# Optimization experiments

Measured on AMD Instinct MI355X. Metric: run time of the kernel, lower is better.

Reference implementation:

```python
import jax, jax.numpy as jnp
import numpy as np

B, L, D = 2, 2048, 1024
H, G = 16, 2            # num_heads, num_kv_groups
HPG = H // G            # heads per kv group = 8
DQK, DV = 128, 128      # qk_head_dim, v_head_dim (head_dim=64, ratios=2.0)


def setup_inputs() -> dict:
    key = jax.random.key(0)
    ks = jax.random.split(key, 12)

    def xavier(k, shape, scale=1.0):
        fan_in, fan_out = shape[0], shape[1]
        lim = np.sqrt(6.0 / (fan_in + fan_out))
        return jax.random.uniform(k, shape, jnp.float32, -lim, lim) * scale

    return {
        "in_q": jax.random.normal(ks[0], (B, L, D), jnp.float32),
        "in_k": jax.random.normal(ks[1], (B, L, D), jnp.float32),
        "in_v": jax.random.normal(ks[2], (B, L, D), jnp.float32),
        # weights stored as [in, out] (transpose of torch Linear); qk_init_scale=0.5
        "Wq": xavier(ks[3], (D, H * DQK), 0.5),
        "bq": jnp.zeros((H * DQK,), jnp.float32),
        "Wk": xavier(ks[4], (D, G * DQK), 0.5),
        "bk": jnp.zeros((G * DQK,), jnp.float32),
        "Wv": xavier(ks[5], (D, G * DV)),
        "bv": jnp.zeros((G * DV,), jnp.float32),
        "Wo": xavier(ks[6], (H * DV, D)),
        "bo": jnp.zeros((D,), jnp.float32),
        "q_extra_scale": jnp.ones((1,), jnp.float32),
    }


def reference(in_q, in_k, in_v, Wq, bq, Wk, bk, Wv, bv, Wo, bo, q_extra_scale):
    # fused projections
    q = (in_q @ Wq + bq) * q_extra_scale              # [B,L,H*DQK]
    k = in_k @ Wk + bk                                 # [B,L,G*DQK]
    v = in_v @ Wv + bv                                 # [B,L,G*DV]

    # reshape: keep GQA group structure instead of materializing repeat_interleave
    q = q.reshape(B, L, G, HPG, DQK)                   # heads grouped: head h = g*HPG + m
    k = k.reshape(B, L, G, DQK)
    v = v.reshape(B, L, G, DV)

    scale = 1.0 / np.sqrt(DQK)
    # scores: [B,G,HPG,L_q,L_kv]
    scores = jnp.einsum("bsgmd,btgd->bgmst", q, k) * scale
    causal = jnp.tril(jnp.ones((L, L), bool))          # is_causal=True
    scores = jnp.where(causal, scores, jnp.finfo(scores.dtype).min)
    attn = jax.nn.softmax(scores, axis=-1)
    ctx = jnp.einsum("bgmst,btgd->bsgmd", attn, v)     # [B,L,G,HPG,DV]
    ctx = ctx.reshape(B, L, H * DV)
    return ctx @ Wo + bo                               # [B,L,D]
```

## Files before the change

### kernel.cpp

```cpp
#include <hip/hip_runtime.h>


typedef __bf16 bf16;
typedef __bf16 bf16x8 __attribute__((ext_vector_type(8)));
typedef __bf16 bf16x4 __attribute__((ext_vector_type(4)));
typedef float f32x4 __attribute__((ext_vector_type(4)));
typedef float float4v __attribute__((ext_vector_type(4)));

#define MFMA_BF16(a, b, c) __builtin_amdgcn_mfma_f32_16x16x32_bf16((a), (b), (c), 0, 0, 0)

static constexpr int Bz = 2, Lz = 2048, Dz = 1024;
static constexpr int Hz = 16, Gz = 2;
static constexpr int DQKz = 128, DVz = 128;

__device__ __forceinline__ void async_copy16(const bf16* g, bf16* l) {
    __builtin_amdgcn_global_load_lds(
        (const __attribute__((address_space(1))) unsigned int*)g,
        (__attribute__((address_space(3))) unsigned int*)l, 16, 0, 0);
}

__global__ __launch_bounds__(256) void cvt3(
    const float* __restrict__ q, const float* __restrict__ k,
    const float* __restrict__ v, bf16* __restrict__ dq,
    bf16* __restrict__ dk, bf16* __restrict__ dv)
{
    const float* s = blockIdx.y == 0 ? q : (blockIdx.y == 1 ? k : v);
    bf16* d = blockIdx.y == 0 ? dq : (blockIdx.y == 1 ? dk : dv);
    int i = (blockIdx.x * 256 + threadIdx.x) * 8;
    float4v a = *(const float4v*)(s + i);
    float4v b = *(const float4v*)(s + i + 4);
    bf16x8 o;
    #pragma unroll
    for (int j = 0; j < 4; ++j) { o[j] = (bf16)a[j]; o[j + 4] = (bf16)b[j]; }
    *(bf16x8*)(d + i) = o;
}

__global__ __launch_bounds__(256) void wtrans4(
    const float* __restrict__ W0, bf16* __restrict__ T0,
    const float* __restrict__ W1, bf16* __restrict__ T1,
    const float* __restrict__ W2, bf16* __restrict__ T2,
    const float* __restrict__ W3, bf16* __restrict__ T3)
{
    const float* W; bf16* WT; int K, N;
    switch (blockIdx.z) {
        case 0:  W = W0; WT = T0; K = 1024; N = 2048; break;
        case 1:  W = W1; WT = T1; K = 1024; N = 256;  break;
        case 2:  W = W2; WT = T2; K = 1024; N = 256;  break;
        default: W = W3; WT = T3; K = 2048; N = 1024; break;
    }
    int tiles_n = N >> 5, tiles_k = K >> 5;
    int linear = blockIdx.x + blockIdx.y * 64;
    if (linear >= tiles_n * tiles_k) return;
    int n0 = (linear % tiles_n) * 32, k0 = (linear / tiles_n) * 32;

    __shared__ bf16 t[32][33];
    int tx = threadIdx.x & 31, ty = threadIdx.x >> 5;
    #pragma unroll
    for (int i = 0; i < 4; ++i)
        t[ty + i * 8][tx] = (bf16)W[(size_t)(k0 + ty + i * 8) * N + n0 + tx];
    __syncthreads();
    #pragma unroll
    for (int i = 0; i < 4; ++i)
        WT[(size_t)(n0 + ty + i * 8) * K + k0 + tx] = t[tx][ty + i * 8];
}

template <typename TC>
__global__ __launch_bounds__(256, 3) void gemm128(
    const bf16* __restrict__ A, const bf16* __restrict__ BT,
    const float* __restrict__ bias, const float* __restrict__ scale_ptr,
    float scale_const, TC* __restrict__ C, int M, int N, int K)
{
    __shared__ bf16 As[128 * 64];
    __shared__ bf16 Bs[128 * 64];

    const int tid  = threadIdx.x;
    const int wave = tid >> 6;
    const int lane = tid & 63;
    const int quad = lane >> 4;
    const int l16  = lane & 15;
    const int sw   = l16 & 7;
    const int wm = wave >> 1, wn = wave & 1;
    const int m0 = blockIdx.y * 128;
    const int n0 = blockIdx.x * 128;

    f32x4 acc[4][4] = {};

    for (int k0 = 0; k0 < K; k0 += 64) {
        #pragma unroll
        for (int s = 0; s < 4; ++s) {
            int i = s * 256 + tid;
            int row = i >> 3, c = (i & 7) ^ (row & 7);
            async_copy16(A + (size_t)(m0 + row) * K + k0 + c * 8, &As[(size_t)i * 8]);
        }
        #pragma unroll
        for (int s = 0; s < 4; ++s) {
            int i = s * 256 + tid;
            int row = i >> 3, c = (i & 7) ^ (row & 7);
            async_copy16(BT + (size_t)(n0 + row) * K + k0 + c * 8, &Bs[(size_t)i * 8]);
        }
        __syncthreads();

        #pragma unroll
        for (int ks = 0; ks < 2; ++ks) {
            bf16x8 af[4], bfv[4];
            #pragma unroll
            for (int mt = 0; mt < 4; ++mt)
                af[mt] = *(const bf16x8*)(&As[((wm * 64 + mt * 16 + l16) * 8
                                               + ((ks * 4 + quad) ^ sw)) * 8]);
            #pragma unroll
            for (int nt = 0; nt < 4; ++nt)
                bfv[nt] = *(const bf16x8*)(&Bs[((wn * 64 + nt * 16 + l16) * 8
                                                + ((ks * 4 + quad) ^ sw)) * 8]);
            #pragma unroll
            for (int mt = 0; mt < 4; ++mt)
                #pragma unroll
                for (int nt = 0; nt < 4; ++nt)
                    acc[mt][nt] = MFMA_BF16(af[mt], bfv[nt], acc[mt][nt]);
        }
        __syncthreads();
    }

    const float scale = (scale_ptr ? scale_ptr[0] : 1.0f) * scale_const;
    #pragma unroll
    for (int nt = 0; nt < 4; ++nt) {
        int col = n0 + wn * 64 + nt * 16 + l16;
        float bv = bias[col];
        #pragma unroll
        for (int mt = 0; mt < 4; ++mt)
            #pragma unroll
            for (int r = 0; r < 4; ++r) {
                int row = m0 + wm * 64 + mt * 16 + quad * 4 + r;
                C[(size_t)row * N + col] = (TC)((acc[mt][nt][r] + bv) * scale);
            }
    }
}

__global__ __launch_bounds__(256, 4) void gemm64_kv(
    const bf16* __restrict__ A0, const bf16* __restrict__ BT0,
    const float* __restrict__ bias0, bf16* __restrict__ C0,
    const bf16* __restrict__ A1, const bf16* __restrict__ BT1,
    const float* __restrict__ bias1, bf16* __restrict__ C1,
    int M, int N, int K)
{
    const bool isV = blockIdx.z == 1;
    const bf16* A  = isV ? A1 : A0;
    const bf16* BT = isV ? BT1 : BT0;
    const float* bias = isV ? bias1 : bias0;
    bf16* C = isV ? C1 : C0;

    __shared__ bf16 As[64 * 64];
    __shared__ bf16 Bs[64 * 64];

    const int tid  = threadIdx.x;
    const int wave = tid >> 6;
    const int lane = tid & 63;
    const int quad = lane >> 4;
    const int l16  = lane & 15;
    const int sw   = l16 & 7;
    const int m0 = blockIdx.y * 64;
    const int n0 = blockIdx.x * 64;

    f32x4 acc[4] = {};

    for (int k0 = 0; k0 < K; k0 += 64) {
        #pragma unroll
        for (int s = 0; s < 2; ++s) {
            int i = s * 256 + tid;
            int row = i >> 3, c = (i & 7) ^ (row & 7);
            async_copy16(A + (size_t)(m0 + row) * K + k0 + c * 8, &As[(size_t)i * 8]);
        }
        #pragma unroll
        for (int s = 0; s < 2; ++s) {
            int i = s * 256 + tid;
            int row = i >> 3, c = (i & 7) ^ (row & 7);
            async_copy16(BT + (size_t)(n0 + row) * K + k0 + c * 8, &Bs[(size_t)i * 8]);
        }
        __syncthreads();

        #pragma unroll
        for (int ks = 0; ks < 2; ++ks) {
            bf16x8 af = *(const bf16x8*)(&As[((wave * 16 + l16) * 8
                                              + ((ks * 4 + quad) ^ sw)) * 8]);
            #pragma unroll
            for (int nf = 0; nf < 4; ++nf) {
                bf16x8 bfv = *(const bf16x8*)(&Bs[((nf * 16 + l16) * 8
                                                   + ((ks * 4 + quad) ^ sw)) * 8]);
                acc[nf] = MFMA_BF16(af, bfv, acc[nf]);
            }
        }
        __syncthreads();
    }

    #pragma unroll
    for (int nf = 0; nf < 4; ++nf) {
        int col = n0 + nf * 16 + l16;
        float bv = bias[col];
        #pragma unroll
        for (int r = 0; r < 4; ++r) {
            int row = m0 + wave * 16 + quad * 4 + r;
            float v = acc[nf][r] + bv;
            if (isV) C[(size_t)col * M + row] = (bf16)v;
            else     C[(size_t)row * N + col] = (bf16)v;
        }
    }
}

__global__ __launch_bounds__(256, 2) void attn_fused(
    const bf16* __restrict__ Q,
    const bf16* __restrict__ Kp,
    const bf16* __restrict__ VT,
    bf16* __restrict__ ctx)
{
    __shared__ bf16 Kb[2][64 * 128];
    __shared__ bf16 Vb[2][128 * 64];
    __shared__ bf16 Ps[4 * 16 * 68];

    const int tid  = threadIdx.x;
    const int wave = tid >> 6;
    const int lane = tid & 63;
    const int quad = lane >> 4;
    const int l16  = lane & 15;
    const int sw   = l16 & 7;

    const int h  = blockIdx.y;
    const int b  = blockIdx.z;
    const int g  = h >> 3;

    const bf16* kgbase = Kp + (size_t)(b * Lz) * (Gz * DQKz) + g * DQKz;
    const bf16* vgbase = VT + (size_t)(g * DVz) * (Bz * Lz) + b * Lz;

    auto stage = [&](int kt, int buf) {
        const bf16* kb = kgbase + (size_t)(kt * 64) * (Gz * DQKz);
        #pragma unroll
        for (int s = 0; s < 4; ++s) {
            int i = s * 256 + tid;
            int key = i >> 4, c = (i & 15) ^ (key & 7);
            async_copy16(kb + (size_t)key * (Gz * DQKz) + c * 8,
                         &Kb[buf][(size_t)i * 8]);
        }
        const bf16* vb = vgbase + kt * 64;
        #pragma unroll
        for (int s = 0; s < 4; ++s) {
            int i = s * 256 + tid;
            int dv = i >> 3, c = (i & 7) ^ (dv & 7);
            async_copy16(vb + (size_t)dv * (Bz * Lz) + c * 8,
                         &Vb[buf][(size_t)i * 8]);
        }
    };

    for (int pass = 0; pass < 2; ++pass) {
        const int qt  = pass == 0 ? (31 - blockIdx.x) : blockIdx.x;
        const int q0  = qt * 64;
        const int nkt = qt + 1;

        bf16x8 qf[4];
        {
            const int qrow = q0 + wave * 16 + l16;
            const bf16* qbase = Q + (size_t)(b * Lz + qrow) * (Hz * DQKz) + h * DQKz;
            #pragma unroll
            for (int ks = 0; ks < 4; ++ks)
                qf[ks] = *(const bf16x8*)(qbase + ks * 32 + quad * 8);
        }

        f32x4 oacc[8] = {};
        float lrow[4] = {0.0f, 0.0f, 0.0f, 0.0f};

        if (pass) __syncthreads();
        stage(0, 0);
        int cur = 0;

        for (int kt = 0; kt < nkt; ++kt) {
            __syncthreads();
            if (kt + 1 < nkt) stage(kt + 1, cur ^ 1);

            const bf16* kcur = Kb[cur];
            const bf16* vcur = Vb[cur];

            f32x4 sacc[4] = {};
            #pragma unroll
            for (int nf = 0; nf < 4; ++nf) {
                #pragma unroll
                for (int ks = 0; ks < 4; ++ks) {
                    bf16x8 kf = *(const bf16x8*)(&kcur[((nf * 16 + l16) * 16
                                                        + ((ks * 4 + quad) ^ sw)) * 8]);
                    sacc[nf] = MFMA_BF16(qf[ks], kf, sacc[nf]);
                }
            }

            float pv[4][4];
            if (kt == nkt - 1) {
                const int kv0 = kt * 64;
                #pragma unroll
                for (int nf = 0; nf < 4; ++nf) {
                    int col = kv0 + nf * 16 + l16;
                    #pragma unroll
                    for (int r = 0; r < 4; ++r) {
                        int row = q0 + wave * 16 + quad * 4 + r;
                        pv[nf][r] = (col > row) ? 0.0f : exp2f(sacc[nf][r] - 8.0f);
                    }
                }
            } else {
                #pragma unroll
                for (int nf = 0; nf < 4; ++nf)
                    #pragma unroll
                    for (int r = 0; r < 4; ++r)
                        pv[nf][r] = exp2f(sacc[nf][r] - 8.0f);
            }

            #pragma unroll
            for (int r = 0; r < 4; ++r)
                lrow[r] += (pv[0][r] + pv[1][r]) + (pv[2][r] + pv[3][r]);

            bf16* ps = &Ps[wave * 16 * 68];
            #pragma unroll
            for (int nf = 0; nf < 4; ++nf)
                #pragma unroll
                for (int r = 0; r < 4; ++r)
                    ps[(quad * 4 + r) * 68 + nf * 16 + l16] = (bf16)pv[nf][r];

            #pragma unroll
            for (int ks2 = 0; ks2 < 2; ++ks2) {
                bf16x4 plo = *(const bf16x4*)(&ps[l16 * 68 + ks2 * 32 + quad * 8]);
                bf16x4 phi = *(const bf16x4*)(&ps[l16 * 68 + ks2 * 32 + quad * 8 + 4]);
                bf16x8 pf;
                #pragma unroll
                for (int i = 0; i < 4; ++i) { pf[i] = plo[i]; pf[i + 4] = phi[i]; }
                #pragma unroll
                for (int nf2 = 0; nf2 < 8; ++nf2) {
                    bf16x8 vf = *(const bf16x8*)(&vcur[((nf2 * 16 + l16) * 8
                                                        + ((ks2 * 4 + quad) ^ sw)) * 8]);
                    oacc[nf2] = MFMA_BF16(pf, vf, oacc[nf2]);
                }
            }
            cur ^= 1;
        }

        #pragma unroll
        for (int r = 0; r < 4; ++r) {
            #pragma unroll
            for (int off = 1; off < 16; off <<= 1)
                lrow[r] += __shfl_xor(lrow[r], off);
        }
        #pragma unroll
        for (int nf2 = 0; nf2 < 8; ++nf2) {
            int col = h * DVz + nf2 * 16 + l16;
            #pragma unroll
            for (int r = 0; r < 4; ++r) {
                int row = q0 + wave * 16 + quad * 4 + r;
                ctx[(size_t)(b * Lz + row) * (Hz * DVz) + col] =
                    (bf16)(oacc[nf2][r] / lrow[r]);
            }
        }
    }
}

extern "C" void kernel_launch(void* const* d_in, const int* in_sizes, int n_in,
                              void* d_out, int out_size, void* d_ws, size_t ws_size,
                              hipStream_t stream)
{
    (void)in_sizes; (void)n_in; (void)out_size; (void)ws_size;

    const float* in_q = (const float*)d_in[0];
    const float* in_k = (const float*)d_in[1];
    const float* in_v = (const float*)d_in[2];
    const float* Wq   = (const float*)d_in[3];
    const float* bq   = (const float*)d_in[4];
    const float* Wk   = (const float*)d_in[5];
    const float* bk   = (const float*)d_in[6];
    const float* Wv   = (const float*)d_in[7];
    const float* bv   = (const float*)d_in[8];
    const float* Wo   = (const float*)d_in[9];
    const float* bo   = (const float*)d_in[10];
    const float* qsc  = (const float*)d_in[11];
    float* out = (float*)d_out;

    const int M = Bz * Lz;
    const int NQ = Hz * DQKz;
    const int NKV = Gz * DQKz;

    bf16* aq  = (bf16*)d_ws;
    bf16* WqT = aq  + (size_t)M * Dz;
    bf16* WkT = WqT + (size_t)NQ * Dz;
    bf16* WvT = WkT + (size_t)NKV * Dz;
    bf16* WoT = WvT + (size_t)NKV * Dz;
    bf16* Qw  = WoT + (size_t)Dz * NQ;
    bf16* Kw  = Qw  + (size_t)M * NQ;
    bf16* VwT = Kw  + (size_t)M * NKV;
    bf16* Cw  = VwT + (size_t)NKV * M;
    bf16* ak  = Cw;
    bf16* av  = Cw + (size_t)M * Dz;

    dim3 blk256(256);

    cvt3<<<dim3((M * Dz) / 2048, 3), blk256, 0, stream>>>(in_q, in_k, in_v, aq, ak, av);
    wtrans4<<<dim3(64, 32, 4), blk256, 0, stream>>>(Wq, WqT, Wk, WkT, Wv, WvT, Wo, WoT);

    const float qscale = 0.08838834764831845f * 1.4426950408889634f;
    gemm128<bf16><<<dim3(NQ / 128, M / 128), blk256, 0, stream>>>(
        aq, WqT, bq, qsc, qscale, Qw, M, NQ, Dz);

    gemm64_kv<<<dim3(NKV / 64, M / 64, 2), blk256, 0, stream>>>(
        ak, WkT, bk, Kw, av, WvT, bv, VwT, M, NKV, Dz);

    attn_fused<<<dim3(Lz / 128, Hz, Bz), blk256, 0, stream>>>(Qw, Kw, VwT, Cw);

    gemm128<float><<<dim3(Dz / 128, M / 128), blk256, 0, stream>>>(
        Cw, WoT, bo, nullptr, 1.0f, out, M, Dz, NQ);
}
```

Measured before the change: 273.3 us.

## Merge prep kernels, fuse QKV projections, double-buffer GEMMs, transpose attention MFMA layout

```diff
diff --git a/kernel.cpp b/kernel.cpp
--- a/kernel.cpp
+++ b/kernel.cpp
@@ -19,39 +19,36 @@
         (__attribute__((address_space(3))) unsigned int*)l, 16, 0, 0);
 }
 
-__global__ __launch_bounds__(256) void cvt3(
+__global__ __launch_bounds__(256) void prep(
     const float* __restrict__ q, const float* __restrict__ k,
     const float* __restrict__ v, bf16* __restrict__ dq,
-    bf16* __restrict__ dk, bf16* __restrict__ dv)
-{
-    const float* s = blockIdx.y == 0 ? q : (blockIdx.y == 1 ? k : v);
-    bf16* d = blockIdx.y == 0 ? dq : (blockIdx.y == 1 ? dk : dv);
-    int i = (blockIdx.x * 256 + threadIdx.x) * 8;
-    float4v a = *(const float4v*)(s + i);
-    float4v b = *(const float4v*)(s + i + 4);
-    bf16x8 o;
-    #pragma unroll
-    for (int j = 0; j < 4; ++j) { o[j] = (bf16)a[j]; o[j + 4] = (bf16)b[j]; }
-    *(bf16x8*)(d + i) = o;
-}
-
-__global__ __launch_bounds__(256) void wtrans4(
-    const float* __restrict__ W0, bf16* __restrict__ T0,
-    const float* __restrict__ W1, bf16* __restrict__ T1,
-    const float* __restrict__ W2, bf16* __restrict__ T2,
-    const float* __restrict__ W3, bf16* __restrict__ T3)
-{
+    bf16* __restrict__ dk, bf16* __restrict__ dv,
+    const float* __restrict__ Wq, const float* __restrict__ Wk,
+    const float* __restrict__ Wv, const float* __restrict__ Wo,
+    bf16* __restrict__ WqT, bf16* __restrict__ WkT,
+    bf16* __restrict__ WvT, bf16* __restrict__ WoT)
+{
+    int bid = blockIdx.x;
+    if (bid < 6144) {
+        const float* s = bid < 2048 ? q : (bid < 4096 ? k : v);
+        bf16* d = bid < 2048 ? dq : (bid < 4096 ? dk : dv);
+        int i = (bid & 2047) * 2048 + threadIdx.x * 8;
+        float4v a = *(const float4v*)(s + i);
+        float4v b = *(const float4v*)(s + i + 4);
+        bf16x8 o;
+        #pragma unroll
+        for (int j = 0; j < 4; ++j) { o[j] = (bf16)a[j]; o[j + 4] = (bf16)b[j]; }
+        *(bf16x8*)(d + i) = o;
+        return;
+    }
+    bid -= 6144;
     const float* W; bf16* WT; int K, N;
-    switch (blockIdx.z) {
-        case 0:  W = W0; WT = T0; K = 1024; N = 2048; break;
-        case 1:  W = W1; WT = T1; K = 1024; N = 256;  break;
-        case 2:  W = W2; WT = T2; K = 1024; N = 256;  break;
-        default: W = W3; WT = T3; K = 2048; N = 1024; break;
-    }
-    int tiles_n = N >> 5, tiles_k = K >> 5;
-    int linear = blockIdx.x + blockIdx.y * 64;
-    if (linear >= tiles_n * tiles_k) return;
-    int n0 = (linear % tiles_n) * 32, k0 = (linear / tiles_n) * 32;
+    if (bid < 2048)      { W = Wq; WT = WqT; K = 1024; N = 2048; }
+    else if (bid < 2304) { W = Wk; WT = WkT; K = 1024; N = 256;  bid -= 2048; }
+    else if (bid < 2560) { W = Wv; WT = WvT; K = 1024; N = 256;  bid -= 2304; }
+    else                 { W = Wo; WT = WoT; K = 2048; N = 1024; bid -= 2560; }
+    int tiles_n = N >> 5;
+    int n0 = (bid % tiles_n) * 32, k0 = (bid / tiles_n) * 32;
 
     __shared__ bf16 t[32][33];
     int tx = threadIdx.x & 31, ty = threadIdx.x >> 5;
@@ -65,91 +62,132 @@
 }
 
 template <typename TC>
-__global__ __launch_bounds__(256, 3) void gemm128(
+__device__ __forceinline__ void gemm_tile(
     const bf16* __restrict__ A, const bf16* __restrict__ BT,
-    const float* __restrict__ bias, const float* __restrict__ scale_ptr,
-    float scale_const, TC* __restrict__ C, int M, int N, int K)
-{
-    __shared__ bf16 As[128 * 64];
-    __shared__ bf16 Bs[128 * 64];
-
+    const float* __restrict__ bias, float scale, TC* __restrict__ C,
+    int M, int N, int K, int m0, int n0, bool trans_out,
+    bf16 (&As)[2][128 * 64], bf16 (&Bs)[2][128 * 64])
+{
     const int tid  = threadIdx.x;
     const int wave = tid >> 6;
     const int lane = tid & 63;
     const int quad = lane >> 4;
     const int l16  = lane & 15;
     const int sw   = l16 & 7;
-    const int wm = wave >> 1, wn = wave & 1;
-    const int m0 = blockIdx.y * 128;
-    const int n0 = blockIdx.x * 128;
-
-    f32x4 acc[4][4] = {};
-
+    const int wm = wave >> 2, wn = wave & 3;
+
+    f32x4 acc[4][2] = {};
+
+    auto stage = [&](int k0, int buf) {
+        #pragma unroll
+        for (int s = 0; s < 2; ++s) {
+            int i = s * 512 + tid;
+            int row = i >> 3, c = (i & 7) ^ (row & 7);
+            async_copy16(A + (size_t)(m0 + row) * K + k0 + c * 8, &As[buf][i * 8]);
+        }
+        #pragma unroll
+        for (int s = 0; s < 2; ++s) {
+            int i = s * 512 + tid;
+            int row = i >> 3, c = (i & 7) ^ (row & 7);
+            async_copy16(BT + (size_t)(n0 + row) * K + k0 + c * 8, &Bs[buf][i * 8]);
+        }
+    };
+
+    stage(0, 0);
+    int cur = 0;
     for (int k0 = 0; k0 < K; k0 += 64) {
-        #pragma unroll
-        for (int s = 0; s < 4; ++s) {
-            int i = s * 256 + tid;
-            int row = i >> 3, c = (i & 7) ^ (row & 7);
-            async_copy16(A + (size_t)(m0 + row) * K + k0 + c * 8, &As[(size_t)i * 8]);
-        }
-        #pragma unroll
-        for (int s = 0; s < 4; ++s) {
-            int i = s * 256 + tid;
-            int row = i >> 3, c = (i & 7) ^ (row & 7);
-            async_copy16(BT + (size_t)(n0 + row) * K + k0 + c * 8, &Bs[(size_t)i * 8]);
-        }
         __syncthreads();
+        if (k0 + 64 < K) stage(k0 + 64, cur ^ 1);
 
         #pragma unroll
         for (int ks = 0; ks < 2; ++ks) {
-            bf16x8 af[4], bfv[4];
+            bf16x8 af[4], bfv[2];
             #pragma unroll
             for (int mt = 0; mt < 4; ++mt)
-                af[mt] = *(const bf16x8*)(&As[((wm * 64 + mt * 16 + l16) * 8
-                                               + ((ks * 4 + quad) ^ sw)) * 8]);
-            #pragma unroll
-            for (int nt = 0; nt < 4; ++nt)
-                bfv[nt] = *(const bf16x8*)(&Bs[((wn * 64 + nt * 16 + l16) * 8
-                                                + ((ks * 4 + quad) ^ sw)) * 8]);
+                af[mt] = *(const bf16x8*)(&As[cur][((wm * 64 + mt * 16 + l16) * 8
+                                                    + ((ks * 4 + quad) ^ sw)) * 8]);
+            #pragma unroll
+            for (int nt = 0; nt < 2; ++nt)
+                bfv[nt] = *(const bf16x8*)(&Bs[cur][((wn * 32 + nt * 16 + l16) * 8
+                                                     + ((ks * 4 + quad) ^ sw)) * 8]);
             #pragma unroll
             for (int mt = 0; mt < 4; ++mt)
                 #pragma unroll
-                for (int nt = 0; nt < 4; ++nt)
+                for (int nt = 0; nt < 2; ++nt)
                     acc[mt][nt] = MFMA_BF16(af[mt], bfv[nt], acc[mt][nt]);
         }
-        __syncthreads();
-    }
-
-    const float scale = (scale_ptr ? scale_ptr[0] : 1.0f) * scale_const;
+        cur ^= 1;
+    }
+
     #pragma unroll
-    for (int nt = 0; nt < 4; ++nt) {
-        int col = n0 + wn * 64 + nt * 16 + l16;
+    for (int nt = 0; nt < 2; ++nt) {
+        int col = n0 + wn * 32 + nt * 16 + l16;
         float bv = bias[col];
         #pragma unroll
-        for (int mt = 0; mt < 4; ++mt)
-            #pragma unroll
-            for (int r = 0; r < 4; ++r) {
-                int row = m0 + wm * 64 + mt * 16 + quad * 4 + r;
-                C[(size_t)row * N + col] = (TC)((acc[mt][nt][r] + bv) * scale);
-            }
-    }
-}
-
-__global__ __launch_bounds__(256, 4) void gemm64_kv(
-    const bf16* __restrict__ A0, const bf16* __restrict__ BT0,
-    const float* __restrict__ bias0, bf16* __restrict__ C0,
-    const bf16* __restrict__ A1, const bf16* __restrict__ BT1,
-    const float* __restrict__ bias1, bf16* __restrict__ C1,
-    int M, int N, int K)
-{
-    const bool isV = blockIdx.z == 1;
-    const bf16* A  = isV ? A1 : A0;
-    const bf16* BT = isV ? BT1 : BT0;
-    const float* bias = isV ? bias1 : bias0;
-    bf16* C = isV ? C1 : C0;
-
-    __shared__ bf16 As[64 * 64];
-    __shared__ bf16 Bs[64 * 64];
+        for (int mt = 0; mt < 4; ++mt) {
+            int row = m0 + wm * 64 + mt * 16 + quad * 4;
+            if (trans_out) {
+                struct V4 { TC v[4]; } o;
+                #pragma unroll
+                for (int r = 0; r < 4; ++r)
+                    o.v[r] = (TC)((acc[mt][nt][r] + bv) * scale);
+                *(V4*)(&C[(size_t)col * M + row]) = o;
+            } else {
+                #pragma unroll
+                for (int r = 0; r < 4; ++r)
+                    C[(size_t)(row + r) * N + col] =
+                        (TC)((acc[mt][nt][r] + bv) * scale);
+            }
+        }
+    }
+}
+
+__global__ __launch_bounds__(512, 4) void proj_qkv(
+    const bf16* __restrict__ aq, const bf16* __restrict__ ak,
+    const bf16* __restrict__ av, const bf16* __restrict__ WqT,
+    const bf16* __restrict__ WkT, const bf16* __restrict__ WvT,
+    const float* __restrict__ bq, const float* __restrict__ bk,
+    const float* __restrict__ bv, const float* __restrict__ qsc,
+    bf16* __restrict__ Qw, bf16* __restrict__ Kw, bf16* __restrict__ VwT)
+{
+    __shared__ bf16 As[2][128 * 64];
+    __shared__ bf16 Bs[2][128 * 64];
+    int bid = blockIdx.x;
+    if (bid < 512) {
+        float scale = qsc[0] * 0.08838834764831845f * 1.4426950408889634f;
+        gemm_tile<bf16>(aq, WqT, bq, scale, Qw, 4096, 2048, 1024,
+                        (bid >> 4) * 128, (bid & 15) * 128, false, As, Bs);
+    } else if (bid < 576) {
+        int b2 = bid - 512;
+        gemm_tile<bf16>(ak, WkT, bk, 1.0f, Kw, 4096, 256, 1024,
+                        (b2 >> 1) * 128, (b2 & 1) * 128, false, As, Bs);
+    } else {
+        int b2 = bid - 576;
+        gemm_tile<bf16>(av, WvT, bv, 1.0f, VwT, 4096, 256, 1024,
+                        (b2 >> 1) * 128, (b2 & 1) * 128, true, As, Bs);
+    }
+}
+
+__global__ __launch_bounds__(512, 4) void proj_o(
+    const bf16* __restrict__ Cw, const bf16* __restrict__ WoT,
+    const float* __restrict__ bo, float* __restrict__ out)
+{
+    __shared__ bf16 As[2][128 * 64];
+    __shared__ bf16 Bs[2][128 * 64];
+    gemm_tile<float>(Cw, WoT, bo, 1.0f, out, 4096, 1024, 2048,
+                     (blockIdx.x >> 3) * 128, (blockIdx.x & 7) * 128,
+                     false, As, Bs);
+}
+
+__global__ __launch_bounds__(256, 2) void attn_fused(
+    const bf16* __restrict__ Q,
+    const bf16* __restrict__ Kp,
+    const bf16* __restrict__ VT,
+    bf16* __restrict__ ctx)
+{
+    __shared__ bf16 Kb[2][64 * 128];
+    __shared__ bf16 Vb[2][128 * 64];
+    __shared__ bf16 Ps[4][16 * 72];
 
     const int tid  = threadIdx.x;
     const int wave = tid >> 6;
@@ -157,74 +195,10 @@
     const int quad = lane >> 4;
     const int l16  = lane & 15;
     const int sw   = l16 & 7;
-    const int m0 = blockIdx.y * 64;
-    const int n0 = blockIdx.x * 64;
-
-    f32x4 acc[4] = {};
-
-    for (int k0 = 0; k0 < K; k0 += 64) {
-        #pragma unroll
-        for (int s = 0; s < 2; ++s) {
-            int i = s * 256 + tid;
-            int row = i >> 3, c = (i & 7) ^ (row & 7);
-            async_copy16(A + (size_t)(m0 + row) * K + k0 + c * 8, &As[(size_t)i * 8]);
-        }
-        #pragma unroll
-        for (int s = 0; s < 2; ++s) {
-            int i = s * 256 + tid;
-            int row = i >> 3, c = (i & 7) ^ (row & 7);
-            async_copy16(BT + (size_t)(n0 + row) * K + k0 + c * 8, &Bs[(size_t)i * 8]);
-        }
-        __syncthreads();
-
-        #pragma unroll
-        for (int ks = 0; ks < 2; ++ks) {
-            bf16x8 af = *(const bf16x8*)(&As[((wave * 16 + l16) * 8
-                                              + ((ks * 4 + quad) ^ sw)) * 8]);
-            #pragma unroll
-            for (int nf = 0; nf < 4; ++nf) {
-                bf16x8 bfv = *(const bf16x8*)(&Bs[((nf * 16 + l16) * 8
-                                                   + ((ks * 4 + quad) ^ sw)) * 8]);
-                acc[nf] = MFMA_BF16(af, bfv, acc[nf]);
-            }
-        }
-        __syncthreads();
-    }
-
-    #pragma unroll
-    for (int nf = 0; nf < 4; ++nf) {
-        int col = n0 + nf * 16 + l16;
-        float bv = bias[col];
-        #pragma unroll
-        for (int r = 0; r < 4; ++r) {
-            int row = m0 + wave * 16 + quad * 4 + r;
-            float v = acc[nf][r] + bv;
-            if (isV) C[(size_t)col * M + row] = (bf16)v;
-            else     C[(size_t)row * N + col] = (bf16)v;
-        }
-    }
-}
-
-__global__ __launch_bounds__(256, 2) void attn_fused(
-    const bf16* __restrict__ Q,
-    const bf16* __restrict__ Kp,
-    const bf16* __restrict__ VT,
-    bf16* __restrict__ ctx)
-{
-    __shared__ bf16 Kb[2][64 * 128];
-    __shared__ bf16 Vb[2][128 * 64];
-    __shared__ bf16 Ps[4 * 16 * 68];
-
-    const int tid  = threadIdx.x;
-    const int wave = tid >> 6;
-    const int lane = tid & 63;
-    const int quad = lane >> 4;
-    const int l16  = lane & 15;
-    const int sw   = l16 & 7;
-
-    const int h  = blockIdx.y;
-    const int b  = blockIdx.z;
-    const int g  = h >> 3;
+
+    const int h = blockIdx.y;
+    const int b = blockIdx.z;
+    const int g = h >> 3;
 
     const bf16* kgbase = Kp + (size_t)(b * Lz) * (Gz * DQKz) + g * DQKz;
     const bf16* vgbase = VT + (size_t)(g * DVz) * (Bz * Lz) + b * Lz;
@@ -235,16 +209,14 @@
         for (int s = 0; s < 4; ++s) {
             int i = s * 256 + tid;
             int key = i >> 4, c = (i & 15) ^ (key & 7);
-            async_copy16(kb + (size_t)key * (Gz * DQKz) + c * 8,
-                         &Kb[buf][(size_t)i * 8]);
+            async_copy16(kb + (size_t)key * (Gz * DQKz) + c * 8, &Kb[buf][i * 8]);
         }
         const bf16* vb = vgbase + kt * 64;
         #pragma unroll
         for (int s = 0; s < 4; ++s) {
             int i = s * 256 + tid;
             int dv = i >> 3, c = (i & 7) ^ (dv & 7);
-            async_copy16(vb + (size_t)dv * (Bz * Lz) + c * 8,
-                         &Vb[buf][(size_t)i * 8]);
+            async_copy16(vb + (size_t)dv * (Bz * Lz) + c * 8, &Vb[buf][i * 8]);
         }
     };
 
@@ -252,10 +224,10 @@
         const int qt  = pass == 0 ? (31 - blockIdx.x) : blockIdx.x;
         const int q0  = qt * 64;
         const int nkt = qt + 1;
+        const int qrow = q0 + wave * 16 + l16;
 
         bf16x8 qf[4];
         {
-            const int qrow = q0 + wave * 16 + l16;
             const bf16* qbase = Q + (size_t)(b * Lz + qrow) * (Hz * DQKz) + h * DQKz;
             #pragma unroll
             for (int ks = 0; ks < 4; ++ks)
@@ -263,12 +235,14 @@
         }
 
         f32x4 oacc[8] = {};
-        float lrow[4] = {0.0f, 0.0f, 0.0f, 0.0f};
+        float lsum = 0.0f;
 
         if (pass) __syncthreads();
         stage(0, 0);
         int cur = 0;
 
+        bf16* ps = Ps[wave];
+
         for (int kt = 0; kt < nkt; ++kt) {
             __syncthreads();
             if (kt + 1 < nkt) stage(kt + 1, cur ^ 1);
@@ -283,7 +257,7 @@
                 for (int ks = 0; ks < 4; ++ks) {
                     bf16x8 kf = *(const bf16x8*)(&kcur[((nf * 16 + l16) * 16
                                                         + ((ks * 4 + quad) ^ sw)) * 8]);
-                    sacc[nf] = MFMA_BF16(qf[ks], kf, sacc[nf]);
+                    sacc[nf] = MFMA_BF16(kf, qf[ks], sacc[nf]);
                 }
             }
 
@@ -292,12 +266,11 @@
                 const int kv0 = kt * 64;
                 #pragma unroll
                 for (int nf = 0; nf < 4; ++nf) {
-                    int col = kv0 + nf * 16 + l16;
+                    int keyb = kv0 + nf * 16 + quad * 4;
                     #pragma unroll
-                    for (int r = 0; r < 4; ++r) {
-                        int row = q0 + wave * 16 + quad * 4 + r;
-                        pv[nf][r] = (col > row) ? 0.0f : exp2f(sacc[nf][r] - 8.0f);
-                    }
+                    for (int r = 0; r < 4; ++r)
+                        pv[nf][r] = (keyb + r > qrow) ? 0.0f
+                                                      : exp2f(sacc[nf][r] - 8.0f);
                 }
             } else {
                 #pragma unroll
@@ -308,48 +281,41 @@
             }
 
             #pragma unroll
-            for (int r = 0; r < 4; ++r)
-                lrow[r] += (pv[0][r] + pv[1][r]) + (pv[2][r] + pv[3][r]);
-
-            bf16* ps = &Ps[wave * 16 * 68];
-            #pragma unroll
             for (int nf = 0; nf < 4; ++nf)
-                #pragma unroll
-                for (int r = 0; r < 4; ++r)
-                    ps[(quad * 4 + r) * 68 + nf * 16 + l16] = (bf16)pv[nf][r];
+                lsum += (pv[nf][0] + pv[nf][1]) + (pv[nf][2] + pv[nf][3]);
+
+            #pragma unroll
+            for (int nf = 0; nf < 4; ++nf) {
+                bf16x4 pk;
+                #pragma unroll
+                for (int r = 0; r < 4; ++r) pk[r] = (bf16)pv[nf][r];
+                *(bf16x4*)(&ps[l16 * 72 + nf * 16 + quad * 4]) = pk;
+            }
 
             #pragma unroll
             for (int ks2 = 0; ks2 < 2; ++ks2) {
-                bf16x4 plo = *(const bf16x4*)(&ps[l16 * 68 + ks2 * 32 + quad * 8]);
-                bf16x4 phi = *(const bf16x4*)(&ps[l16 * 68 + ks2 * 32 + quad * 8 + 4]);
-                bf16x8 pf;
-                #pragma unroll
-                for (int i = 0; i < 4; ++i) { pf[i] = plo[i]; pf[i + 4] = phi[i]; }
+                bf16x8 pf = *(const bf16x8*)(&ps[l16 * 72 + ks2 * 32 + quad * 8]);
                 #pragma unroll
                 for (int nf2 = 0; nf2 < 8; ++nf2) {
                     bf16x8 vf = *(const bf16x8*)(&vcur[((nf2 * 16 + l16) * 8
                                                         + ((ks2 * 4 + quad) ^ sw)) * 8]);
-                    oacc[nf2] = MFMA_BF16(pf, vf, oacc[nf2]);
+                    oacc[nf2] = MFMA_BF16(vf, pf, oacc[nf2]);
                 }
             }
             cur ^= 1;
         }
 
-        #pragma unroll
-        for (int r = 0; r < 4; ++r) {
-            #pragma unroll
-            for (int off = 1; off < 16; off <<= 1)
-                lrow[r] += __shfl_xor(lrow[r], off);
-        }
+        lsum += __shfl_xor(lsum, 16);
+        lsum += __shfl_xor(lsum, 32);
+        const float inv = 1.0f / lsum;
+
+        bf16* cbase = ctx + (size_t)(b * Lz + qrow) * (Hz * DVz) + h * DVz;
         #pragma unroll
         for (int nf2 = 0; nf2 < 8; ++nf2) {
-            int col = h * DVz + nf2 * 16 + l16;
-            #pragma unroll
-            for (int r = 0; r < 4; ++r) {
-                int row = q0 + wave * 16 + quad * 4 + r;
-                ctx[(size_t)(b * Lz + row) * (Hz * DVz) + col] =
-                    (bf16)(oacc[nf2][r] / lrow[r]);
-            }
+            bf16x4 o4;
+            #pragma unroll
+            for (int r = 0; r < 4; ++r) o4[r] = (bf16)(oacc[nf2][r] * inv);
+            *(bf16x4*)(&cbase[nf2 * 16 + quad * 4]) = o4;
         }
     }
 }
@@ -390,20 +356,13 @@
     bf16* ak  = Cw;
     bf16* av  = Cw + (size_t)M * Dz;
 
-    dim3 blk256(256);
-
-    cvt3<<<dim3((M * Dz) / 2048, 3), blk256, 0, stream>>>(in_q, in_k, in_v, aq, ak, av);
-    wtrans4<<<dim3(64, 32, 4), blk256, 0, stream>>>(Wq, WqT, Wk, WkT, Wv, WvT, Wo, WoT);
-
-    const float qscale = 0.08838834764831845f * 1.4426950408889634f;
-    gemm128<bf16><<<dim3(NQ / 128, M / 128), blk256, 0, stream>>>(
-        aq, WqT, bq, qsc, qscale, Qw, M, NQ, Dz);
-
-    gemm64_kv<<<dim3(NKV / 64, M / 64, 2), blk256, 0, stream>>>(
-        ak, WkT, bk, Kw, av, WvT, bv, VwT, M, NKV, Dz);
-
-    attn_fused<<<dim3(Lz / 128, Hz, Bz), blk256, 0, stream>>>(Qw, Kw, VwT, Cw);
-
-    gemm128<float><<<dim3(Dz / 128, M / 128), blk256, 0, stream>>>(
-        Cw, WoT, bo, nullptr, 1.0f, out, M, Dz, NQ);
-}
+    prep<<<dim3(10752), dim3(256), 0, stream>>>(
+        in_q, in_k, in_v, aq, ak, av, Wq, Wk, Wv, Wo, WqT, WkT, WvT, WoT);
+
+    proj_qkv<<<dim3(640), dim3(512), 0, stream>>>(
+        aq, ak, av, WqT, WkT, WvT, bq, bk, bv, qsc, Qw, Kw, VwT);
+
+    attn_fused<<<dim3(Lz / 128, Hz, Bz), dim3(256), 0, stream>>>(Qw, Kw, VwT, Cw);
+
+    proj_o<<<dim3(256), dim3(512), 0, stream>>>(Cw, WoT, bo, out);
+}
```

Result: faster. 256.4 us (-6.2%).
